# Performance work log

Measured on AMD Instinct MI355X. Metric: run time of the kernel, lower is better.

The kernel has to match this reference:

```python
import jax, jax.numpy as jnp
import numpy as np

# irreps layout: list of (multiplicity, l); same for input and output (square Linear)
IRREPS = [(256, 0), (128, 1), (64, 2)]  # dims: 256 + 384 + 320 = 960
N_NODES = 100000
N_TRIVIAL = 256  # dim of leading 0e block in irreps_out


def setup_inputs() -> dict:
    key = jax.random.key(0)
    ks = jax.random.split(key, 5)
    data_in = jax.random.normal(ks[0], (N_NODES, sum(m * (2 * l + 1) for m, l in IRREPS)), dtype=jnp.float32)
    # weight init matching linear_layer_init: uniform(-a, a), a = sqrt(6/(mul1*mul2 + mul_out)),
    # here mul1 = mul_out = mul, mul2 = 1 -> a = sqrt(6 / (2*mul)) = sqrt(3/mul)
    Ws = {}
    for i, (mul, l) in enumerate(IRREPS):
        a = float(np.sqrt(3.0 / mul))
        Ws[f"W{i}"] = jax.random.uniform(ks[i + 1], (mul, mul), minval=-a, maxval=a, dtype=jnp.float32)
    b = jnp.zeros((N_TRIVIAL,), dtype=jnp.float32)
    return {"data_in": data_in, "W0": Ws["W0"], "W1": Ws["W1"], "W2": Ws["W2"], "b": b}


def reference(data_in, W0, W1, W2, b):
    # FullyConnectedTensorProduct(irreps_in, '1x0e', irreps_out) with x2 = ones reduces to
    # per-irrep block matmul: out_block = (x_block @ W) / sqrt(mul_in)
    # (w3j(l,0,l) = I/sqrt(2l+1) cancels with component-norm sqrt((2l+1)/mul_in)).
    Ws = [W0, W1, W2]
    outs = []
    off = 0
    for (mul, l), W in zip(IRREPS, Ws):
        d = 2 * l + 1
        x = data_in[:, off : off + mul * d].reshape(-1, mul, d)  # [N, mul, 2l+1]
        y = jnp.einsum("bud,uw->bwd", x, W) * (1.0 / np.sqrt(mul))
        outs.append(y.reshape(-1, mul * d))
        off += mul * d
    out = jnp.concatenate(outs, axis=1)
    # bias added only to the leading trivial (0e) block
    out = out.at[:, :N_TRIVIAL].add(b)
    return out
```

## Files before the change

kernel.cpp:

```cpp
#include <hip/hip_runtime.h>

typedef __attribute__((ext_vector_type(8))) short short8;
typedef __attribute__((ext_vector_type(4))) float f32x4;

__device__ __forceinline__ unsigned pack2bf(float x0, float x1) {
    unsigned u0 = __float_as_uint(x0) + 0x8000u;
    unsigned u1 = __float_as_uint(x1) + 0x8000u;
    return __builtin_amdgcn_perm(u1, u0, 0x07060302u);
}

__device__ __forceinline__ void prep_one(const float* __restrict__ W,
                                         unsigned short* __restrict__ dst,
                                         int mul, int shift, float scale, int idx) {
    if (idx >= mul * mul) return;
    int u = idx >> shift;
    int w = idx - (u << shift);
    int nkb = mul >> 5;
    int cb = w >> 4, kb = u >> 5;
    int lane = ((u >> 3) & 3) * 16 + (w & 15);
    int j = u & 7;
    unsigned uv = __float_as_uint(W[idx] * scale) + 0x8000u;
    dst[(((cb * nkb + kb) * 64 + lane) << 3) + j] = (unsigned short)(uv >> 16);
}

__global__ __launch_bounds__(256) void prep_all(const float* __restrict__ W0,
                                                const float* __restrict__ W1,
                                                const float* __restrict__ W2,
                                                unsigned short* __restrict__ wf) {
    int b = blockIdx.x;
    if (b < 256)      prep_one(W0, wf,         256, 8, 0.0625f,              b * 256 + threadIdx.x);
    else if (b < 320) prep_one(W1, wf + 65536, 128, 7, 0.08838834764831845f, (b - 256) * 256 + threadIdx.x);
    else              prep_one(W2, wf + 81920, 64,  6, 0.125f,               (b - 320) * 256 + threadIdx.x);
}

template <int D>
__device__ __forceinline__ void pack_from_lds(const float* __restrict__ lrow, int xr, int c0,
                                              short8* __restrict__ out) {
    float buf[8 * D];
#pragma unroll
    for (int v = 0; v < 2 * D; ++v) {
        f32x4 t = *reinterpret_cast<const f32x4*>(lrow + (((c0 + v) ^ xr) << 2));
        buf[v * 4 + 0] = t[0]; buf[v * 4 + 1] = t[1];
        buf[v * 4 + 2] = t[2]; buf[v * 4 + 3] = t[3];
    }
#pragma unroll
    for (int d = 0; d < D; ++d) {
        union { short8 s8; unsigned u[4]; } fr;
#pragma unroll
        for (int jj = 0; jj < 4; ++jj)
            fr.u[jj] = pack2bf(buf[(2 * jj) * D + d], buf[(2 * jj + 1) * D + d]);
        out[d] = fr.s8;
    }
}

__global__ __launch_bounds__(256, 1) void lin_main(const float* __restrict__ in,
                                                   const unsigned short* __restrict__ wf0,
                                                   const unsigned short* __restrict__ wf1,
                                                   const unsigned short* __restrict__ wf2,
                                                   const float* __restrict__ bias,
                                                   float* __restrict__ out) {
    __shared__ float lds[2][15360];
    const int w = threadIdx.x >> 6;
    const int lane = threadIdx.x & 63;
    const int lm = lane & 15, lg = lane >> 4, xr = lm & 7;

    short8 b0[4][8], b1[2][4], b2[2];
#pragma unroll
    for (int c = 0; c < 4; ++c)
#pragma unroll
        for (int kb = 0; kb < 8; ++kb)
            b0[c][kb] = *reinterpret_cast<const short8*>(wf0 + ((((w * 4 + c) * 8 + kb) * 64 + lane) << 3));
#pragma unroll
    for (int c = 0; c < 2; ++c)
#pragma unroll
        for (int kb = 0; kb < 4; ++kb)
            b1[c][kb] = *reinterpret_cast<const short8*>(wf1 + ((((w * 2 + c) * 4 + kb) * 64 + lane) << 3));
#pragma unroll
    for (int kb = 0; kb < 2; ++kb)
        b2[kb] = *reinterpret_cast<const short8*>(wf2 + (((w * 2 + kb) * 64 + lane) << 3));
    float bv[4];
#pragma unroll
    for (int c = 0; c < 4; ++c) bv[c] = bias[(w * 4 + c) * 16 + lm];

    int srcoff[15];
#pragma unroll
    for (int i = 0; i < 15; ++i) {
        int s = w * 960 + i * 64 + lane;
        int row = (int)(((long long)s * 17477) >> 22);
        int c = s - row * 240;
        srcoff[i] = (row * 240 + (c ^ (row & 7))) << 4;
    }

    const int b = blockIdx.x;
    const int nt = (b < 106) ? 25 : 24;
    const int t0 = b * 24 + (b < 106 ? b : 106);

#define STAGE(kk, bufi)                                                                   \
    {                                                                                     \
        const char* tb = (const char*)in + (size_t)(t0 + (kk)) * 61440;                   \
        char* sd = (char*)&lds[0][0] + (bufi) * 61440 + w * 15360;                        \
        _Pragma("unroll")                                                                 \
        for (int i = 0; i < 15; ++i)                                                      \
            __builtin_amdgcn_global_load_lds(                                             \
                (const __attribute__((address_space(1))) void*)(tb + srcoff[i]),          \
                (__attribute__((address_space(3))) void*)(sd + i * 1024), 16, 0, 0);      \
    }

    STAGE(0, 0);

    for (int k = 0; k < nt; ++k) {
        const int par = k & 1;
        if (k + 1 < nt) {
            STAGE(k + 1, par ^ 1);
            asm volatile("s_waitcnt vmcnt(15)" ::: "memory");
        } else {
            asm volatile("s_waitcnt vmcnt(0)" ::: "memory");
        }
        __builtin_amdgcn_s_barrier();
        __builtin_amdgcn_sched_barrier(0);

        const float* lrow = &lds[0][0] + par * 15360 + lm * 960;
        const int trow = (t0 + k) * 16;
        {
            short8 a[8];
#pragma unroll
            for (int kb = 0; kb < 8; ++kb)
                pack_from_lds<1>(lrow, xr, 8 * kb + 2 * lg, &a[kb]);
#pragma unroll
            for (int c = 0; c < 4; ++c) {
                f32x4 acc = {0.f, 0.f, 0.f, 0.f};
#pragma unroll
                for (int kb = 0; kb < 8; ++kb)
                    acc = __builtin_amdgcn_mfma_f32_16x16x32_bf16(a[kb], b0[c][kb], acc, 0, 0, 0);
#pragma unroll
                for (int jj = 0; jj < 4; ++jj)
                    out[(size_t)(trow + lg * 4 + jj) * 960 + (w * 4 + c) * 16 + lm] = acc[jj] + bv[c];
            }
        }
        {
            short8 a[4][3];
#pragma unroll
            for (int kb = 0; kb < 4; ++kb)
                pack_from_lds<3>(lrow, xr, 64 + 24 * kb + 6 * lg, a[kb]);
#pragma unroll
            for (int c = 0; c < 2; ++c) {
                f32x4 acc[3];
#pragma unroll
                for (int d = 0; d < 3; ++d) acc[d] = (f32x4){0.f, 0.f, 0.f, 0.f};
#pragma unroll
                for (int kb = 0; kb < 4; ++kb)
#pragma unroll
                    for (int d = 0; d < 3; ++d)
                        acc[d] = __builtin_amdgcn_mfma_f32_16x16x32_bf16(a[kb][d], b1[c][kb], acc[d], 0, 0, 0);
#pragma unroll
                for (int jj = 0; jj < 4; ++jj) {
                    float* op = out + (size_t)(trow + lg * 4 + jj) * 960 + 256 + ((w * 2 + c) * 16 + lm) * 3;
#pragma unroll
                    for (int d = 0; d < 3; ++d) op[d] = acc[d][jj];
                }
            }
        }
        {
            short8 a[2][5];
#pragma unroll
            for (int kb = 0; kb < 2; ++kb)
                pack_from_lds<5>(lrow, xr, 160 + 40 * kb + 10 * lg, a[kb]);
            f32x4 acc[5];
#pragma unroll
            for (int d = 0; d < 5; ++d) acc[d] = (f32x4){0.f, 0.f, 0.f, 0.f};
#pragma unroll
            for (int kb = 0; kb < 2; ++kb)
#pragma unroll
                for (int d = 0; d < 5; ++d)
                    acc[d] = __builtin_amdgcn_mfma_f32_16x16x32_bf16(a[kb][d], b2[kb], acc[d], 0, 0, 0);
#pragma unroll
            for (int jj = 0; jj < 4; ++jj) {
                float* op = out + (size_t)(trow + lg * 4 + jj) * 960 + 640 + (w * 16 + lm) * 5;
#pragma unroll
                for (int d = 0; d < 5; ++d) op[d] = acc[d][jj];
            }
        }

        __builtin_amdgcn_sched_barrier(0);
        __builtin_amdgcn_s_barrier();
    }
#undef STAGE
}

extern "C" void kernel_launch(void* const* d_in, const int* in_sizes, int n_in,
                              void* d_out, int out_size, void* d_ws, size_t ws_size,
                              hipStream_t stream) {
    (void)in_sizes; (void)n_in; (void)out_size; (void)ws_size;
    const float* x  = (const float*)d_in[0];
    const float* W0 = (const float*)d_in[1];
    const float* W1 = (const float*)d_in[2];
    const float* W2 = (const float*)d_in[3];
    const float* b  = (const float*)d_in[4];
    float* out = (float*)d_out;
    unsigned short* wf = (unsigned short*)d_ws;

    prep_all<<<336, 256, 0, stream>>>(W0, W1, W2, wf);
    lin_main<<<256, 256, 0, stream>>>(x, wf, wf + 65536, wf + 81920, b, out);
}
```

Before: 168.9 us.

## Restructure pipeline wait to overlap prefetch with compute and use inline-asm stores

Each iteration now issues the prefetch of the next tile, computes all three irrep blocks, and only then waits with vmcnt(60) so the outstanding loads can complete behind the compute and stores. This moves the wait from before compute to after it. All outputs are gathered and written through inline-asm global_store_dword with immediate offsets to cut address arithmetic. The vmcnt accounting relies on exactly 60 stores per iteration and holds all accumulators live at once, which raises register pressure.

```diff
diff --git a/kernel.cpp b/kernel.cpp
--- a/kernel.cpp
+++ b/kernel.cpp
@@ -53,6 +53,9 @@
     }
 }
 
+#define ST(p, val, imm) \
+    asm volatile("global_store_dword %0, %1, off offset:" imm :: "v"(p), "v"(val) : "memory")
+
 __global__ __launch_bounds__(256, 1) void lin_main(const float* __restrict__ in,
                                                    const unsigned short* __restrict__ wf0,
                                                    const unsigned short* __restrict__ wf1,
@@ -107,82 +110,87 @@
     }
 
     STAGE(0, 0);
+    asm volatile("s_waitcnt vmcnt(0)" ::: "memory");
+    __builtin_amdgcn_s_barrier();
+    __builtin_amdgcn_sched_barrier(0);
 
     for (int k = 0; k < nt; ++k) {
         const int par = k & 1;
-        if (k + 1 < nt) {
-            STAGE(k + 1, par ^ 1);
-            asm volatile("s_waitcnt vmcnt(15)" ::: "memory");
-        } else {
-            asm volatile("s_waitcnt vmcnt(0)" ::: "memory");
+        if (k + 1 < nt) STAGE(k + 1, par ^ 1);
+
+        const float* lrow = &lds[0][0] + par * 15360 + lm * 960;
+        const int trow = (t0 + k) * 16;
+
+        short8 a0[8];
+#pragma unroll
+        for (int kb = 0; kb < 8; ++kb)
+            pack_from_lds<1>(lrow, xr, 8 * kb + 2 * lg, &a0[kb]);
+        f32x4 acc0[4];
+#pragma unroll
+        for (int c = 0; c < 4; ++c) {
+            f32x4 z = {0.f, 0.f, 0.f, 0.f};
+#pragma unroll
+            for (int kb = 0; kb < 8; ++kb)
+                z = __builtin_amdgcn_mfma_f32_16x16x32_bf16(a0[kb], b0[c][kb], z, 0, 0, 0);
+            acc0[c] = z;
         }
+        short8 a1[4][3];
+#pragma unroll
+        for (int kb = 0; kb < 4; ++kb)
+            pack_from_lds<3>(lrow, xr, 64 + 24 * kb + 6 * lg, a1[kb]);
+        f32x4 acc1[2][3];
+#pragma unroll
+        for (int c = 0; c < 2; ++c)
+#pragma unroll
+            for (int d = 0; d < 3; ++d) {
+                f32x4 z = {0.f, 0.f, 0.f, 0.f};
+#pragma unroll
+                for (int kb = 0; kb < 4; ++kb)
+                    z = __builtin_amdgcn_mfma_f32_16x16x32_bf16(a1[kb][d], b1[c][kb], z, 0, 0, 0);
+                acc1[c][d] = z;
+            }
+        short8 a2[2][5];
+#pragma unroll
+        for (int kb = 0; kb < 2; ++kb)
+            pack_from_lds<5>(lrow, xr, 160 + 40 * kb + 10 * lg, a2[kb]);
+        f32x4 acc2[5];
+#pragma unroll
+        for (int d = 0; d < 5; ++d) {
+            f32x4 z = {0.f, 0.f, 0.f, 0.f};
+#pragma unroll
+            for (int kb = 0; kb < 2; ++kb)
+                z = __builtin_amdgcn_mfma_f32_16x16x32_bf16(a2[kb][d], b2[kb], z, 0, 0, 0);
+            acc2[d] = z;
+        }
+
+#pragma unroll
+        for (int jj = 0; jj < 4; ++jj) {
+            float* r = out + (size_t)(trow + lg * 4 + jj) * 960;
+            float* p0 = r + w * 64 + lm;
+            ST(p0, acc0[0][jj] + bv[0], "0");
+            ST(p0, acc0[1][jj] + bv[1], "64");
+            ST(p0, acc0[2][jj] + bv[2], "128");
+            ST(p0, acc0[3][jj] + bv[3], "192");
+            float* p1 = r + 256 + (w * 32 + lm) * 3;
+            ST(p1, acc1[0][0][jj], "0");
+            ST(p1, acc1[0][1][jj], "4");
+            ST(p1, acc1[0][2][jj], "8");
+            ST(p1, acc1[1][0][jj], "192");
+            ST(p1, acc1[1][1][jj], "196");
+            ST(p1, acc1[1][2][jj], "200");
+            float* p2 = r + 640 + (w * 16 + lm) * 5;
+            ST(p2, acc2[0][jj], "0");
+            ST(p2, acc2[1][jj], "4");
+            ST(p2, acc2[2][jj], "8");
+            ST(p2, acc2[3][jj], "12");
+            ST(p2, acc2[4][jj], "16");
+        }
+
+        __builtin_amdgcn_sched_barrier(0);
+        if (k + 1 < nt)
+            asm volatile("s_waitcnt vmcnt(60)" ::: "memory");
         __builtin_amdgcn_s_barrier();
         __builtin_amdgcn_sched_barrier(0);
-
-        const float* lrow = &lds[0][0] + par * 15360 + lm * 960;
-        const int trow = (t0 + k) * 16;
-        {
-            short8 a[8];
-#pragma unroll
-            for (int kb = 0; kb < 8; ++kb)
-                pack_from_lds<1>(lrow, xr, 8 * kb + 2 * lg, &a[kb]);
-#pragma unroll
-            for (int c = 0; c < 4; ++c) {
-                f32x4 acc = {0.f, 0.f, 0.f, 0.f};
-#pragma unroll
-                for (int kb = 0; kb < 8; ++kb)
-                    acc = __builtin_amdgcn_mfma_f32_16x16x32_bf16(a[kb], b0[c][kb], acc, 0, 0, 0);
-#pragma unroll
-                for (int jj = 0; jj < 4; ++jj)
-                    out[(size_t)(trow + lg * 4 + jj) * 960 + (w * 4 + c) * 16 + lm] = acc[jj] + bv[c];
-            }
-        }
-        {
-            short8 a[4][3];
-#pragma unroll
-            for (int kb = 0; kb < 4; ++kb)
-                pack_from_lds<3>(lrow, xr, 64 + 24 * kb + 6 * lg, a[kb]);
-#pragma unroll
-            for (int c = 0; c < 2; ++c) {
-                f32x4 acc[3];
-#pragma unroll
-                for (int d = 0; d < 3; ++d) acc[d] = (f32x4){0.f, 0.f, 0.f, 0.f};
-#pragma unroll
-                for (int kb = 0; kb < 4; ++kb)
-#pragma unroll
-                    for (int d = 0; d < 3; ++d)
-                        acc[d] = __builtin_amdgcn_mfma_f32_16x16x32_bf16(a[kb][d], b1[c][kb], acc[d], 0, 0, 0);
-#pragma unroll
-                for (int jj = 0; jj < 4; ++jj) {
-                    float* op = out + (size_t)(trow + lg * 4 + jj) * 960 + 256 + ((w * 2 + c) * 16 + lm) * 3;
-#pragma unroll
-                    for (int d = 0; d < 3; ++d) op[d] = acc[d][jj];
-                }
-            }
-        }
-        {
-            short8 a[2][5];
-#pragma unroll
-            for (int kb = 0; kb < 2; ++kb)
-                pack_from_lds<5>(lrow, xr, 160 + 40 * kb + 10 * lg, a[kb]);
-            f32x4 acc[5];
-#pragma unroll
-            for (int d = 0; d < 5; ++d) acc[d] = (f32x4){0.f, 0.f, 0.f, 0.f};
-#pragma unroll
-            for (int kb = 0; kb < 2; ++kb)
-#pragma unroll
-                for (int d = 0; d < 5; ++d)
-                    acc[d] = __builtin_amdgcn_mfma_f32_16x16x32_bf16(a[kb][d], b2[kb], acc[d], 0, 0, 0);
-#pragma unroll
-            for (int jj = 0; jj < 4; ++jj) {
-                float* op = out + (size_t)(trow + lg * 4 + jj) * 960 + 640 + (w * 16 + lm) * 5;
-#pragma unroll
-                for (int d = 0; d < 5; ++d) op[d] = acc[d][jj];
-            }
-        }
-
-        __builtin_amdgcn_sched_barrier(0);
-        __builtin_amdgcn_s_barrier();
     }
 #undef STAGE
 }
```

Measured after the change: 171.7 us. Within noise of the previous version (+1.7%).

## Split linear into l0/l1 LDS-staged kernel and separate direct-load l2 kernel

Applied to the files above, without the earlier changes.

Splits the fused kernel in two. The first handles the l=0 and l=1 blocks with 512-thread blocks, two blocks per CU, and a smaller LDS footprint, and writes its stores through inline-asm global_store_dword with immediate offsets. The second handles the l=2 block with direct global vector loads and no LDS staging, across 1024 blocks. The aim is better occupancy and overlap, at the cost of an extra launch and a non-coalesced strided read of the l=2 columns.

```diff
diff --git a/kernel.cpp b/kernel.cpp
--- a/kernel.cpp
+++ b/kernel.cpp
@@ -34,6 +34,18 @@
 }
 
 template <int D>
+__device__ __forceinline__ void pack_core(const float* __restrict__ buf, short8* __restrict__ out) {
+#pragma unroll
+    for (int d = 0; d < D; ++d) {
+        union { short8 s8; unsigned u[4]; } fr;
+#pragma unroll
+        for (int jj = 0; jj < 4; ++jj)
+            fr.u[jj] = pack2bf(buf[(2 * jj) * D + d], buf[(2 * jj + 1) * D + d]);
+        out[d] = fr.s8;
+    }
+}
+
+template <int D>
 __device__ __forceinline__ void pack_from_lds(const float* __restrict__ lrow, int xr, int c0,
                                               short8* __restrict__ out) {
     float buf[8 * D];
@@ -43,52 +55,42 @@
         buf[v * 4 + 0] = t[0]; buf[v * 4 + 1] = t[1];
         buf[v * 4 + 2] = t[2]; buf[v * 4 + 3] = t[3];
     }
-#pragma unroll
-    for (int d = 0; d < D; ++d) {
-        union { short8 s8; unsigned u[4]; } fr;
-#pragma unroll
-        for (int jj = 0; jj < 4; ++jj)
-            fr.u[jj] = pack2bf(buf[(2 * jj) * D + d], buf[(2 * jj + 1) * D + d]);
-        out[d] = fr.s8;
-    }
-}
-
-__global__ __launch_bounds__(256, 1) void lin_main(const float* __restrict__ in,
-                                                   const unsigned short* __restrict__ wf0,
-                                                   const unsigned short* __restrict__ wf1,
-                                                   const unsigned short* __restrict__ wf2,
-                                                   const float* __restrict__ bias,
-                                                   float* __restrict__ out) {
-    __shared__ float lds[2][15360];
+    pack_core<D>(buf, out);
+}
+
+#define ST1(p, val, imm) \
+    asm volatile("global_store_dword %0, %1, off offset:" imm :: "v"(p), "v"(val) : "memory")
+
+__global__ __launch_bounds__(512, 2) void lin_ab(const float* __restrict__ in,
+                                                 const unsigned short* __restrict__ wf0,
+                                                 const unsigned short* __restrict__ wf1,
+                                                 const float* __restrict__ bias,
+                                                 float* __restrict__ out) {
+    __shared__ float lds[2][10240];
     const int w = threadIdx.x >> 6;
     const int lane = threadIdx.x & 63;
     const int lm = lane & 15, lg = lane >> 4, xr = lm & 7;
 
-    short8 b0[4][8], b1[2][4], b2[2];
-#pragma unroll
-    for (int c = 0; c < 4; ++c)
+    short8 b0[2][8], b1[4];
+#pragma unroll
+    for (int c = 0; c < 2; ++c)
 #pragma unroll
         for (int kb = 0; kb < 8; ++kb)
-            b0[c][kb] = *reinterpret_cast<const short8*>(wf0 + ((((w * 4 + c) * 8 + kb) * 64 + lane) << 3));
-#pragma unroll
-    for (int c = 0; c < 2; ++c)
-#pragma unroll
-        for (int kb = 0; kb < 4; ++kb)
-            b1[c][kb] = *reinterpret_cast<const short8*>(wf1 + ((((w * 2 + c) * 4 + kb) * 64 + lane) << 3));
-#pragma unroll
-    for (int kb = 0; kb < 2; ++kb)
-        b2[kb] = *reinterpret_cast<const short8*>(wf2 + (((w * 2 + kb) * 64 + lane) << 3));
-    float bv[4];
-#pragma unroll
-    for (int c = 0; c < 4; ++c) bv[c] = bias[(w * 4 + c) * 16 + lm];
-
-    int srcoff[15];
-#pragma unroll
-    for (int i = 0; i < 15; ++i) {
-        int s = w * 960 + i * 64 + lane;
-        int row = (int)(((long long)s * 17477) >> 22);
-        int c = s - row * 240;
-        srcoff[i] = (row * 240 + (c ^ (row & 7))) << 4;
+            b0[c][kb] = *reinterpret_cast<const short8*>(wf0 + ((((w * 2 + c) * 8 + kb) * 64 + lane) << 3));
+#pragma unroll
+    for (int kb = 0; kb < 4; ++kb)
+        b1[kb] = *reinterpret_cast<const short8*>(wf1 + (((w * 4 + kb) * 64 + lane) << 3));
+    float bv[2];
+#pragma unroll
+    for (int c = 0; c < 2; ++c) bv[c] = bias[(w * 2 + c) * 16 + lm];
+
+    int srcoff[5];
+#pragma unroll
+    for (int i = 0; i < 5; ++i) {
+        int s = w * 320 + i * 64 + lane;
+        int row = (int)((s * 26215u) >> 22);
+        int c = s - row * 160;
+        srcoff[i] = row * 3840 + ((c ^ (row & 7)) << 4);
     }
 
     const int b = blockIdx.x;
@@ -98,93 +100,121 @@
 #define STAGE(kk, bufi)                                                                   \
     {                                                                                     \
         const char* tb = (const char*)in + (size_t)(t0 + (kk)) * 61440;                   \
-        char* sd = (char*)&lds[0][0] + (bufi) * 61440 + w * 15360;                        \
+        char* sd = (char*)&lds[0][0] + (bufi) * 40960 + w * 5120;                         \
         _Pragma("unroll")                                                                 \
-        for (int i = 0; i < 15; ++i)                                                      \
+        for (int i = 0; i < 5; ++i)                                                       \
             __builtin_amdgcn_global_load_lds(                                             \
                 (const __attribute__((address_space(1))) void*)(tb + srcoff[i]),          \
                 (__attribute__((address_space(3))) void*)(sd + i * 1024), 16, 0, 0);      \
     }
 
     STAGE(0, 0);
+    asm volatile("s_waitcnt vmcnt(0)" ::: "memory");
+    __builtin_amdgcn_s_barrier();
+    __builtin_amdgcn_sched_barrier(0);
 
     for (int k = 0; k < nt; ++k) {
         const int par = k & 1;
-        if (k + 1 < nt) {
-            STAGE(k + 1, par ^ 1);
-            asm volatile("s_waitcnt vmcnt(15)" ::: "memory");
-        } else {
-            asm volatile("s_waitcnt vmcnt(0)" ::: "memory");
-        }
+        if (k + 1 < nt) STAGE(k + 1, par ^ 1);
+
+        const float* lrow = &lds[0][0] + par * 10240 + lm * 640;
+        const int trow = (t0 + k) * 16;
+
+        short8 a0[8];
+#pragma unroll
+        for (int kb = 0; kb < 8; ++kb)
+            pack_from_lds<1>(lrow, xr, 8 * kb + 2 * lg, &a0[kb]);
+        f32x4 acc0[2];
+#pragma unroll
+        for (int c = 0; c < 2; ++c) {
+            f32x4 z = {0.f, 0.f, 0.f, 0.f};
+#pragma unroll
+            for (int kb = 0; kb < 8; ++kb)
+                z = __builtin_amdgcn_mfma_f32_16x16x32_bf16(a0[kb], b0[c][kb], z, 0, 0, 0);
+            acc0[c] = z;
+        }
+        short8 a1[4][3];
+#pragma unroll
+        for (int kb = 0; kb < 4; ++kb)
+            pack_from_lds<3>(lrow, xr, 64 + 24 * kb + 6 * lg, a1[kb]);
+        f32x4 acc1[3];
+#pragma unroll
+        for (int d = 0; d < 3; ++d) {
+            f32x4 z = {0.f, 0.f, 0.f, 0.f};
+#pragma unroll
+            for (int kb = 0; kb < 4; ++kb)
+                z = __builtin_amdgcn_mfma_f32_16x16x32_bf16(a1[kb][d], b1[kb], z, 0, 0, 0);
+            acc1[d] = z;
+        }
+
+#pragma unroll
+        for (int jj = 0; jj < 4; ++jj) {
+            float* r = out + (size_t)(trow + lg * 4 + jj) * 960;
+            float* p0 = r + w * 32 + lm;
+            ST1(p0, acc0[0][jj] + bv[0], "0");
+            ST1(p0, acc0[1][jj] + bv[1], "64");
+            float* p1 = r + 256 + (w * 16 + lm) * 3;
+            ST1(p1, acc1[0][jj], "0");
+            ST1(p1, acc1[1][jj], "4");
+            ST1(p1, acc1[2][jj], "8");
+        }
+
+        __builtin_amdgcn_sched_barrier(0);
+        if (k + 1 < nt)
+            asm volatile("s_waitcnt vmcnt(20)" ::: "memory");
         __builtin_amdgcn_s_barrier();
         __builtin_amdgcn_sched_barrier(0);
-
-        const float* lrow = &lds[0][0] + par * 15360 + lm * 960;
-        const int trow = (t0 + k) * 16;
-        {
-            short8 a[8];
-#pragma unroll
-            for (int kb = 0; kb < 8; ++kb)
-                pack_from_lds<1>(lrow, xr, 8 * kb + 2 * lg, &a[kb]);
-#pragma unroll
-            for (int c = 0; c < 4; ++c) {
-                f32x4 acc = {0.f, 0.f, 0.f, 0.f};
-#pragma unroll
-                for (int kb = 0; kb < 8; ++kb)
-                    acc = __builtin_amdgcn_mfma_f32_16x16x32_bf16(a[kb], b0[c][kb], acc, 0, 0, 0);
-#pragma unroll
-                for (int jj = 0; jj < 4; ++jj)
-                    out[(size_t)(trow + lg * 4 + jj) * 960 + (w * 4 + c) * 16 + lm] = acc[jj] + bv[c];
+    }
+#undef STAGE
+}
+
+__global__ __launch_bounds__(256, 2) void lin_c(const float* __restrict__ in,
+                                                const unsigned short* __restrict__ wf2,
+                                                float* __restrict__ out) {
+    const int w = threadIdx.x >> 6;
+    const int lane = threadIdx.x & 63;
+    const int lm = lane & 15, lg = lane >> 4;
+
+    short8 b2[4][2];
+#pragma unroll
+    for (int c = 0; c < 4; ++c)
+#pragma unroll
+        for (int kb = 0; kb < 2; ++kb)
+            b2[c][kb] = *reinterpret_cast<const short8*>(wf2 + (((c * 2 + kb) * 64 + lane) << 3));
+
+    for (int t = blockIdx.x * 4 + w; t < 6250; t += 4096) {
+        const float* rp = in + (size_t)t * 15360 + lm * 960 + 640;
+        short8 a2[2][5];
+#pragma unroll
+        for (int kb = 0; kb < 2; ++kb) {
+            float buf[40];
+            const float* p = rp + (kb * 32 + lg * 8) * 5;
+#pragma unroll
+            for (int v = 0; v < 10; ++v) {
+                f32x4 x = *reinterpret_cast<const f32x4*>(p + v * 4);
+                buf[v * 4 + 0] = x[0]; buf[v * 4 + 1] = x[1];
+                buf[v * 4 + 2] = x[2]; buf[v * 4 + 3] = x[3];
             }
-        }
-        {
-            short8 a[4][3];
-#pragma unroll
-            for (int kb = 0; kb < 4; ++kb)
-                pack_from_lds<3>(lrow, xr, 64 + 24 * kb + 6 * lg, a[kb]);
-#pragma unroll
-            for (int c = 0; c < 2; ++c) {
-                f32x4 acc[3];
-#pragma unroll
-                for (int d = 0; d < 3; ++d) acc[d] = (f32x4){0.f, 0.f, 0.f, 0.f};
-#pragma unroll
-                for (int kb = 0; kb < 4; ++kb)
-#pragma unroll
-                    for (int d = 0; d < 3; ++d)
-                        acc[d] = __builtin_amdgcn_mfma_f32_16x16x32_bf16(a[kb][d], b1[c][kb], acc[d], 0, 0, 0);
-#pragma unroll
-                for (int jj = 0; jj < 4; ++jj) {
-                    float* op = out + (size_t)(trow + lg * 4 + jj) * 960 + 256 + ((w * 2 + c) * 16 + lm) * 3;
-#pragma unroll
-                    for (int d = 0; d < 3; ++d) op[d] = acc[d][jj];
-                }
-            }
-        }
-        {
-            short8 a[2][5];
+            pack_core<5>(buf, a2[kb]);
+        }
+#pragma unroll
+        for (int c = 0; c < 4; ++c) {
+            f32x4 acc[5];
+#pragma unroll
+            for (int d = 0; d < 5; ++d) acc[d] = (f32x4){0.f, 0.f, 0.f, 0.f};
 #pragma unroll
             for (int kb = 0; kb < 2; ++kb)
-                pack_from_lds<5>(lrow, xr, 160 + 40 * kb + 10 * lg, a[kb]);
-            f32x4 acc[5];
-#pragma unroll
-            for (int d = 0; d < 5; ++d) acc[d] = (f32x4){0.f, 0.f, 0.f, 0.f};
-#pragma unroll
-            for (int kb = 0; kb < 2; ++kb)
 #pragma unroll
                 for (int d = 0; d < 5; ++d)
-                    acc[d] = __builtin_amdgcn_mfma_f32_16x16x32_bf16(a[kb][d], b2[kb], acc[d], 0, 0, 0);
+                    acc[d] = __builtin_amdgcn_mfma_f32_16x16x32_bf16(a2[kb][d], b2[c][kb], acc[d], 0, 0, 0);
 #pragma unroll
             for (int jj = 0; jj < 4; ++jj) {
-                float* op = out + (size_t)(trow + lg * 4 + jj) * 960 + 640 + (w * 16 + lm) * 5;
+                float* op = out + (size_t)(t * 16 + lg * 4 + jj) * 960 + 640 + (c * 16 + lm) * 5;
 #pragma unroll
                 for (int d = 0; d < 5; ++d) op[d] = acc[d][jj];
             }
         }
-
-        __builtin_amdgcn_sched_barrier(0);
-        __builtin_amdgcn_s_barrier();
-    }
-#undef STAGE
+    }
 }
 
 extern "C" void kernel_launch(void* const* d_in, const int* in_sizes, int n_in,
@@ -200,5 +230,6 @@
     unsigned short* wf = (unsigned short*)d_ws;
 
     prep_all<<<336, 256, 0, stream>>>(W0, W1, W2, wf);
-    lin_main<<<256, 256, 0, stream>>>(x, wf, wf + 65536, wf + 81920, b, out);
-}
+    lin_ab<<<256, 512, 0, stream>>>(x, wf, wf + 65536, b, out);
+    lin_c<<<1024, 256, 0, stream>>>(x, wf + 81920, out);
+}
```

New measurement: 194.4 us. 1.15x slower.
